# Optimization experiments

Hardware: AMD Instinct MI355X
Metric: run time of the kernel (lower is better)

Reference implementation:

```python
import jax, jax.numpy as jnp
import numpy as np

N = 50000
E = 800000
IN_C, HID_C, OUT_C = 128, 256, 128
BN_EPS = 1e-5


def glorot(key, shape):
    fan_in, fan_out = shape
    lim = float(np.sqrt(6.0 / (fan_in + fan_out)))
    return jax.random.uniform(key, shape, jnp.float32, -lim, lim)


def setup_inputs() -> dict:
    key = jax.random.key(0)
    ks = jax.random.split(key, 16)
    inp = {
        "x": jax.random.normal(ks[0], (N, IN_C), jnp.float32),
        "edge_index": jax.random.randint(ks[1], (2, E), 0, N, jnp.int64),
        # SAGEConv 1 (in->hid): lin_l has bias, lin_r has no bias (PyG default)
        "wl1": glorot(ks[2], (IN_C, HID_C)), "bl1": jnp.zeros((HID_C,), jnp.float32),
        "wr1": glorot(ks[3], (IN_C, HID_C)),
        # SAGEConv 2 (hid->hid)
        "wl2": glorot(ks[4], (HID_C, HID_C)), "bl2": jnp.zeros((HID_C,), jnp.float32),
        "wr2": glorot(ks[5], (HID_C, HID_C)),
        # SAGEConv 3 (hid->out)
        "wl3": glorot(ks[6], (HID_C, OUT_C)), "bl3": jnp.zeros((OUT_C,), jnp.float32),
        "wr3": glorot(ks[7], (HID_C, OUT_C)),
        # BatchNorm params (eval mode: running stats)
        "bn1_w": jnp.ones((HID_C,), jnp.float32), "bn1_b": jnp.zeros((HID_C,), jnp.float32),
        "bn1_m": jax.random.normal(ks[8], (HID_C,), jnp.float32) * 0.1,
        "bn1_v": jax.random.uniform(ks[9], (HID_C,), jnp.float32, 0.5, 1.5),
        "bn2_w": jnp.ones((HID_C,), jnp.float32), "bn2_b": jnp.zeros((HID_C,), jnp.float32),
        "bn2_m": jax.random.normal(ks[10], (HID_C,), jnp.float32) * 0.1,
        "bn2_v": jax.random.uniform(ks[11], (HID_C,), jnp.float32, 0.5, 1.5),
    }
    return inp


def sage_conv(x, src, dst, wl, bl, wr):
    # mean aggregation of source-node features at destination nodes
    agg = jax.ops.segment_sum(x[src], dst, num_segments=N)          # [N, d_in]
    deg = jax.ops.segment_sum(jnp.ones((E,), x.dtype), dst, num_segments=N)
    mean = agg / jnp.maximum(deg, 1.0)[:, None]
    return mean @ wl + bl + x @ wr                                   # [N, d_out]


def batch_norm(x, w, b, m, v):
    return (x - m) * jax.lax.rsqrt(v + BN_EPS) * w + b


def reference(x, edge_index, wl1, bl1, wr1, wl2, bl2, wr2, wl3, bl3, wr3,
              bn1_w, bn1_b, bn1_m, bn1_v, bn2_w, bn2_b, bn2_m, bn2_v):
    src, dst = edge_index[0], edge_index[1]
    # layer 1: SAGEConv -> BN -> ReLU (dropout is identity in eval mode)
    h = sage_conv(x, src, dst, wl1, bl1, wr1)
    h = jax.nn.relu(batch_norm(h, bn1_w, bn1_b, bn1_m, bn1_v))
    # layer 2
    h = sage_conv(h, src, dst, wl2, bl2, wr2)
    h = jax.nn.relu(batch_norm(h, bn2_w, bn2_b, bn2_m, bn2_v))
    # output layer: plain SAGEConv
    return sage_conv(h, src, dst, wl3, bl3, wr3)
```

## Files before the change

### kernel.cpp

```cpp
#include <hip/hip_runtime.h>
#include <hip/hip_bf16.h>

#define NN 50000
#define NE 800000
#define AGG_BLOCKS 2048

typedef __attribute__((ext_vector_type(8))) short bh8;
typedef __attribute__((ext_vector_type(4))) float f32x4;

static __device__ __forceinline__ unsigned short f2bf(float f){
  unsigned u = __float_as_uint(f);
  unsigned r = (u + 0x7fffu + ((u >> 16) & 1u)) >> 16;
  return (unsigned short)r;
}
static __device__ __forceinline__ float bflo(unsigned u){ return __uint_as_float(u << 16); }
static __device__ __forceinline__ float bfhi(unsigned u){ return __uint_as_float(u & 0xffff0000u); }
static __device__ __forceinline__ unsigned packbf2(float lo, float hi){
  return ((unsigned)f2bf(hi) << 16) | (unsigned)f2bf(lo);
}
static __device__ __forceinline__ unsigned char f2fp8(float v){
  return (unsigned char)(__builtin_amdgcn_cvt_pk_fp8_f32(v, v, 0, false) & 0xff);
}

static __device__ __forceinline__ void gload16(const void* g, void* l){
  __builtin_amdgcn_global_load_lds(
      (const __attribute__((address_space(1))) unsigned int*)g,
      (__attribute__((address_space(3))) unsigned int*)l, 16, 0, 0);
}

__global__ __launch_bounds__(256) void pre_k(
    const int* __restrict__ srcv, const int* __restrict__ dstv,
    int* __restrict__ cnt, int* __restrict__ cslot,
    const float4* __restrict__ x, uint2* __restrict__ xb, unsigned* __restrict__ xq,
    const float* __restrict__ wl1, const float* __restrict__ wr1,
    const float* __restrict__ wl2, const float* __restrict__ wr2,
    const float* __restrict__ wl3, const float* __restrict__ wr3,
    const float* __restrict__ bl1, const float* __restrict__ bl2,
    const float* __restrict__ bn1w, const float* __restrict__ bn1b,
    const float* __restrict__ bn1m, const float* __restrict__ bn1v,
    const float* __restrict__ bn2w, const float* __restrict__ bn2b,
    const float* __restrict__ bn2m, const float* __restrict__ bn2v,
    unsigned short* __restrict__ B1t, unsigned short* __restrict__ B2t,
    unsigned short* __restrict__ B3t,
    float* __restrict__ S1, float* __restrict__ T1,
    float* __restrict__ S2, float* __restrict__ T2)
{
  const int blk = blockIdx.x;
  if (blk < 1024){
    const int part  = blk & 3;
    const int chunk = blk >> 2;
    const int lo = part * (NN / 4);
    const int hi = lo + (NN / 4);
    const int base = chunk * (NE / 256);
    const int endi = base + (NE / 256);
    for (int i = base + threadIdx.x; i < endi; i += 256){
      int d = dstv[i];
      if (d >= lo && d < hi){
        int p = atomicAdd(&cnt[d], 1);
        if (p < 64) cslot[(d << 6) + p] = srcv[i];
      }
    }
  } else if (blk < 2050){
    int i = (blk - 1024) * 256 + threadIdx.x;
    if (i < 65536){
      int n = i >> 8, k = i & 255;
      float v = (k < 128) ? wl1[k * 256 + n] : wr1[(k - 128) * 256 + n];
      B1t[n * 256 + k] = f2bf(v);
    } else if (i < 65536 + 131072){
      int j = i - 65536; int n = j >> 9, k = j & 511;
      float v = (k < 256) ? wl2[k * 256 + n] : wr2[(k - 256) * 256 + n];
      B2t[n * 512 + k] = f2bf(v);
    } else if (i < 65536 + 131072 + 65536){
      int j = i - (65536 + 131072); int n = j >> 8, k = j & 255;
      float v = (n < 128) ? wl3[k * 128 + n] : wr3[k * 128 + (n - 128)];
      B3t[n * 256 + k] = f2bf(v);
    } else if (i < 65536 + 131072 + 65536 + 512){
      int j = i - (65536 + 131072 + 65536);
      if (j < 256){
        float s = bn1w[j] * rsqrtf(bn1v[j] + 1e-5f);
        S1[j] = s; T1[j] = (bl1[j] - bn1m[j]) * s + bn1b[j];
      } else {
        int c = j - 256;
        float s = bn2w[c] * rsqrtf(bn2v[c] + 1e-5f);
        S2[c] = s; T2[c] = (bl2[c] - bn2m[c]) * s + bn2b[c];
      }
    }
  } else {
    int i = (blk - 2050) * 256 + threadIdx.x;
    if (i < NN * 128 / 4){
      float4 v = x[i];
      uint2 o; o.x = packbf2(v.x, v.y); o.y = packbf2(v.z, v.w);
      xb[i] = o;
      int w = 0;
      w = __builtin_amdgcn_cvt_pk_fp8_f32(v.x, v.y, w, false);
      w = __builtin_amdgcn_cvt_pk_fp8_f32(v.z, v.w, w, true);
      xq[i] = (unsigned)w;
    }
  }
}

__global__ __launch_bounds__(256) void agg128q_k(const unsigned short* __restrict__ featq,
                         unsigned* __restrict__ out,
                         const int* __restrict__ cnt, const int* __restrict__ cslot){
  const int lane = threadIdx.x & 63;
  const int node0 = __builtin_amdgcn_readfirstlane(blockIdx.x * 4 + (threadIdx.x >> 6));
  const int nw = gridDim.x * 4;
  for (int node = node0; node < NN; node += nw){
    const int start = node << 6;
    const int deg0 = cnt[node];
    const int deg = deg0 < 64 ? deg0 : 64;
    const int end = start + deg;
    float a0 = 0.f, a1 = 0.f, b0 = 0.f, b1 = 0.f;
    int e = start;
    for (; e + 7 < end; e += 8){
      unsigned u0 = featq[(size_t)cslot[e]     * 64 + lane];
      unsigned u1 = featq[(size_t)cslot[e + 1] * 64 + lane];
      unsigned u2 = featq[(size_t)cslot[e + 2] * 64 + lane];
      unsigned u3 = featq[(size_t)cslot[e + 3] * 64 + lane];
      unsigned u4 = featq[(size_t)cslot[e + 4] * 64 + lane];
      unsigned u5 = featq[(size_t)cslot[e + 5] * 64 + lane];
      unsigned u6 = featq[(size_t)cslot[e + 6] * 64 + lane];
      unsigned u7 = featq[(size_t)cslot[e + 7] * 64 + lane];
      a0 += __builtin_amdgcn_cvt_f32_fp8(u0, 0); a1 += __builtin_amdgcn_cvt_f32_fp8(u0, 1);
      b0 += __builtin_amdgcn_cvt_f32_fp8(u1, 0); b1 += __builtin_amdgcn_cvt_f32_fp8(u1, 1);
      a0 += __builtin_amdgcn_cvt_f32_fp8(u2, 0); a1 += __builtin_amdgcn_cvt_f32_fp8(u2, 1);
      b0 += __builtin_amdgcn_cvt_f32_fp8(u3, 0); b1 += __builtin_amdgcn_cvt_f32_fp8(u3, 1);
      a0 += __builtin_amdgcn_cvt_f32_fp8(u4, 0); a1 += __builtin_amdgcn_cvt_f32_fp8(u4, 1);
      b0 += __builtin_amdgcn_cvt_f32_fp8(u5, 0); b1 += __builtin_amdgcn_cvt_f32_fp8(u5, 1);
      a0 += __builtin_amdgcn_cvt_f32_fp8(u6, 0); a1 += __builtin_amdgcn_cvt_f32_fp8(u6, 1);
      b0 += __builtin_amdgcn_cvt_f32_fp8(u7, 0); b1 += __builtin_amdgcn_cvt_f32_fp8(u7, 1);
    }
    for (; e < end; ++e){
      unsigned u = featq[(size_t)cslot[e] * 64 + lane];
      a0 += __builtin_amdgcn_cvt_f32_fp8(u, 0); a1 += __builtin_amdgcn_cvt_f32_fp8(u, 1);
    }
    float inv = 1.f / (float)(deg0 > 0 ? deg0 : 1);
    out[(size_t)node * 64 + lane] = packbf2((a0 + b0) * inv, (a1 + b1) * inv);
  }
}

#define DEC8(u, x0, x1, x2, x3) { \
  x0 += __builtin_amdgcn_cvt_f32_fp8((u), 0); \
  x1 += __builtin_amdgcn_cvt_f32_fp8((u), 1); \
  x2 += __builtin_amdgcn_cvt_f32_fp8((u), 2); \
  x3 += __builtin_amdgcn_cvt_f32_fp8((u), 3); }

__global__ __launch_bounds__(256) void agg256q_k(const unsigned* __restrict__ featq, unsigned* __restrict__ out,
                         const int* __restrict__ cnt, const int* __restrict__ cslot){
  const int lane = threadIdx.x & 63;
  const int node0 = __builtin_amdgcn_readfirstlane(blockIdx.x * 4 + (threadIdx.x >> 6));
  const int nw = gridDim.x * 4;
  for (int node = node0; node < NN; node += nw){
    const int start = node << 6;
    const int deg0 = cnt[node];
    const int deg = deg0 < 64 ? deg0 : 64;
    const int end = start + deg;
    float a0 = 0.f, a1 = 0.f, a2 = 0.f, a3 = 0.f;
    float b0 = 0.f, b1 = 0.f, b2 = 0.f, b3 = 0.f;
    int e = start;
    for (; e + 7 < end; e += 8){
      unsigned u0 = featq[(size_t)cslot[e]     * 64 + lane];
      unsigned u1 = featq[(size_t)cslot[e + 1] * 64 + lane];
      unsigned u2 = featq[(size_t)cslot[e + 2] * 64 + lane];
      unsigned u3 = featq[(size_t)cslot[e + 3] * 64 + lane];
      unsigned u4 = featq[(size_t)cslot[e + 4] * 64 + lane];
      unsigned u5 = featq[(size_t)cslot[e + 5] * 64 + lane];
      unsigned u6 = featq[(size_t)cslot[e + 6] * 64 + lane];
      unsigned u7 = featq[(size_t)cslot[e + 7] * 64 + lane];
      DEC8(u0, a0, a1, a2, a3) DEC8(u1, b0, b1, b2, b3)
      DEC8(u2, a0, a1, a2, a3) DEC8(u3, b0, b1, b2, b3)
      DEC8(u4, a0, a1, a2, a3) DEC8(u5, b0, b1, b2, b3)
      DEC8(u6, a0, a1, a2, a3) DEC8(u7, b0, b1, b2, b3)
    }
    for (; e < end; ++e){
      unsigned u = featq[(size_t)cslot[e] * 64 + lane];
      DEC8(u, a0, a1, a2, a3)
    }
    float inv = 1.f / (float)(deg0 > 0 ? deg0 : 1);
    uint2 o; o.x = packbf2((a0 + b0) * inv, (a1 + b1) * inv);
    o.y = packbf2((a2 + b2) * inv, (a3 + b3) * inv);
    *reinterpret_cast<uint2*>(out + (size_t)node * 128 + lane * 2) = o;
  }
}

__global__ __launch_bounds__(256) void final_k(const unsigned short* __restrict__ tq,
                        const unsigned* __restrict__ ub, float* __restrict__ out,
                        const int* __restrict__ cnt, const int* __restrict__ cslot,
                        const float* __restrict__ bl3){
  const int lane = threadIdx.x & 63;
  const int node0 = __builtin_amdgcn_readfirstlane(blockIdx.x * 4 + (threadIdx.x >> 6));
  const int nw = gridDim.x * 4;
  for (int node = node0; node < NN; node += nw){
    const int start = node << 6;
    const int deg0 = cnt[node];
    const int deg = deg0 < 64 ? deg0 : 64;
    const int end = start + deg;
    float a0 = 0.f, a1 = 0.f, b0 = 0.f, b1 = 0.f;
    int e = start;
    for (; e + 7 < end; e += 8){
      unsigned u0 = tq[(size_t)cslot[e]     * 64 + lane];
      unsigned u1 = tq[(size_t)cslot[e + 1] * 64 + lane];
      unsigned u2 = tq[(size_t)cslot[e + 2] * 64 + lane];
      unsigned u3 = tq[(size_t)cslot[e + 3] * 64 + lane];
      unsigned u4 = tq[(size_t)cslot[e + 4] * 64 + lane];
      unsigned u5 = tq[(size_t)cslot[e + 5] * 64 + lane];
      unsigned u6 = tq[(size_t)cslot[e + 6] * 64 + lane];
      unsigned u7 = tq[(size_t)cslot[e + 7] * 64 + lane];
      a0 += __builtin_amdgcn_cvt_f32_fp8(u0, 0); a1 += __builtin_amdgcn_cvt_f32_fp8(u0, 1);
      b0 += __builtin_amdgcn_cvt_f32_fp8(u1, 0); b1 += __builtin_amdgcn_cvt_f32_fp8(u1, 1);
      a0 += __builtin_amdgcn_cvt_f32_fp8(u2, 0); a1 += __builtin_amdgcn_cvt_f32_fp8(u2, 1);
      b0 += __builtin_amdgcn_cvt_f32_fp8(u3, 0); b1 += __builtin_amdgcn_cvt_f32_fp8(u3, 1);
      a0 += __builtin_amdgcn_cvt_f32_fp8(u4, 0); a1 += __builtin_amdgcn_cvt_f32_fp8(u4, 1);
      b0 += __builtin_amdgcn_cvt_f32_fp8(u5, 0); b1 += __builtin_amdgcn_cvt_f32_fp8(u5, 1);
      a0 += __builtin_amdgcn_cvt_f32_fp8(u6, 0); a1 += __builtin_amdgcn_cvt_f32_fp8(u6, 1);
      b0 += __builtin_amdgcn_cvt_f32_fp8(u7, 0); b1 += __builtin_amdgcn_cvt_f32_fp8(u7, 1);
    }
    for (; e < end; ++e){
      unsigned u = tq[(size_t)cslot[e] * 64 + lane];
      a0 += __builtin_amdgcn_cvt_f32_fp8(u, 0); a1 += __builtin_amdgcn_cvt_f32_fp8(u, 1);
    }
    float inv = 1.f / (float)(deg0 > 0 ? deg0 : 1);
    unsigned uw = ub[(size_t)node * 64 + lane];
    float2 v;
    v.x = bflo(uw) + (a0 + b0) * inv + bl3[lane * 2];
    v.y = bfhi(uw) + (a1 + b1) * inv + bl3[lane * 2 + 1];
    *(reinterpret_cast<float2*>(out + (size_t)node * 128) + lane) = v;
  }
}

template<int KTOT, int K0, int MODE>
__global__ __launch_bounds__(256) void gemm_k(
    const unsigned short* __restrict__ A0, const unsigned short* __restrict__ A1,
    const unsigned short* __restrict__ Bt,
    const float* __restrict__ S, const float* __restrict__ Tt,
    unsigned short* __restrict__ outB, unsigned char* __restrict__ outQ,
    float* __restrict__ outF, int M)
{
  __shared__ __align__(16) unsigned char lds[49152];
  const int tid = threadIdx.x;
  const int lane = tid & 63;
  const int wv = tid >> 6;
  const int wm = wv >> 1, wn = wv & 1;

  const int nwg = gridDim.x;
  const int q = nwg >> 3, r8 = nwg & 7;
  const int xcd = blockIdx.x & 7, idx = blockIdx.x >> 3;
  const int wg = (xcd < r8) ? xcd * (q + 1) + idx : r8 * (q + 1) + (xcd - r8) * q + idx;
  const int bm = wg >> 1, bn = wg & 1;

  const int rr0 = tid >> 2,         g0 = (tid & 3) ^ ((tid >> 3) & 3);
  const int rr1 = (tid + 256) >> 2, g1 = ((tid + 256) & 3) ^ (((tid + 256) >> 3) & 3);
  int growA0 = bm * 128 + rr0; if (growA0 > M - 1) growA0 = M - 1;
  int growA1 = bm * 128 + rr1; if (growA1 > M - 1) growA1 = M - 1;
  const size_t browA0 = (size_t)(bn * 128 + rr0) * KTOT;
  const size_t browA1 = (size_t)(bn * 128 + rr1) * KTOT;

  const int l15 = lane & 15, kg = lane >> 4;
  const int slot = (kg ^ ((l15 >> 1) & 3)) * 16;

  constexpr int NT = KTOT / 32;

  auto STAGE = [&](int buf, int kt){
    const int kb = kt * 32;
    const unsigned short* Ap; int pitch, kk;
    if (KTOT == K0 || kb < K0){ Ap = A0; pitch = K0; kk = kb; }
    else { Ap = A1; pitch = KTOT - K0; kk = kb - K0; }
    unsigned char* base = lds + buf * 16384;
    gload16(Ap + (size_t)growA0 * pitch + kk + g0 * 8, base + tid * 16);
    gload16(Ap + (size_t)growA1 * pitch + kk + g1 * 8, base + 4096 + tid * 16);
    gload16(Bt + browA0 + kb + g0 * 8, base + 8192 + tid * 16);
    gload16(Bt + browA1 + kb + g1 * 8, base + 12288 + tid * 16);
  };

  f32x4 acc[4][4];
  #pragma unroll
  for (int i = 0; i < 4; ++i)
    #pragma unroll
    for (int j = 0; j < 4; ++j){ acc[i][j][0]=0.f; acc[i][j][1]=0.f; acc[i][j][2]=0.f; acc[i][j][3]=0.f; }

  STAGE(0, 0);
  if (NT > 1) STAGE(1, 1);

  int rb = 0, sb = 2;
  for (int kt = 0; kt < NT; ++kt){
    if (kt < NT - 1) asm volatile("s_waitcnt vmcnt(4)" ::: "memory");
    else             asm volatile("s_waitcnt vmcnt(0)" ::: "memory");
    __builtin_amdgcn_s_barrier();
    __builtin_amdgcn_sched_barrier(0);

    if (kt + 2 < NT){ STAGE(sb, kt + 2); sb = (sb == 2) ? 0 : sb + 1; }

    unsigned char* base = lds + rb * 16384;
    rb = (rb == 2) ? 0 : rb + 1;

    bh8 af[4], bf[4];
    #pragma unroll
    for (int mi = 0; mi < 4; ++mi){
      int rA = wm * 64 + mi * 16 + l15;
      af[mi] = *reinterpret_cast<const bh8*>(base + rA * 64 + slot);
    }
    #pragma unroll
    for (int ni = 0; ni < 4; ++ni){
      int rB = wn * 64 + ni * 16 + l15;
      bf[ni] = *reinterpret_cast<const bh8*>(base + 8192 + rB * 64 + slot);
    }
    __builtin_amdgcn_s_setprio(1);
    #pragma unroll
    for (int mi = 0; mi < 4; ++mi)
      #pragma unroll
      for (int ni = 0; ni < 4; ++ni)
        acc[mi][ni] = __builtin_amdgcn_mfma_f32_16x16x32_bf16(af[mi], bf[ni], acc[mi][ni], 0, 0, 0);
    __builtin_amdgcn_s_setprio(0);
  }

  #pragma unroll
  for (int mi = 0; mi < 4; ++mi){
    int rbase = bm * 128 + wm * 64 + mi * 16 + ((lane >> 4) << 2);
    #pragma unroll
    for (int ni = 0; ni < 4; ++ni){
      int col = bn * 128 + wn * 64 + ni * 16 + (lane & 15);
      #pragma unroll
      for (int j = 0; j < 4; ++j){
        int row = rbase + j;
        if (row < M){
          float v = acc[mi][ni][j];
          if (MODE == 0){
            v = v * S[col] + Tt[col];
            v = v > 0.f ? v : 0.f;
            outB[(size_t)row * 256 + col] = f2bf(v);
            if (outQ) outQ[(size_t)row * 256 + col] = f2fp8(v);
          } else {
            if (col < 128) outQ[(size_t)row * 128 + col] = f2fp8(v);
            else           outF[(size_t)row * 128 + (col - 128)] = v;
          }
        }
      }
    }
  }
}

__global__ __launch_bounds__(256) void gemm23_k(
    const unsigned short* __restrict__ A0 ,
    const unsigned short* __restrict__ A1 ,
    const unsigned short* __restrict__ B2 ,
    const unsigned short* __restrict__ B3 ,
    const float* __restrict__ S, const float* __restrict__ Tt,
    unsigned char* __restrict__ tq, unsigned short* __restrict__ ub, int M)
{
  __shared__ __align__(16) unsigned char lds[61440];
  const int tid = threadIdx.x;
  const int lane = tid & 63;
  const int wv = tid >> 6;

  const int nwg = gridDim.x;
  const int q = nwg >> 3, r8 = nwg & 7;
  const int xcd = blockIdx.x & 7, idx = blockIdx.x >> 3;
  const int bm = (xcd < r8) ? xcd * (q + 1) + idx : r8 * (q + 1) + (xcd - r8) * q + idx;

  const int l15 = lane & 15, kg = lane >> 4;
  const int slot = (kg ^ ((l15 >> 1) & 3)) * 16;
  const int rr = tid >> 2;
  const int g  = (tid & 3) ^ ((tid >> 3) & 3);
  int grow = bm * 64 + rr; if (grow > M - 1) grow = M - 1;

  auto STAGE = [&](int buf, int kt){
    const int kb = kt * 32;
    const unsigned short* Ap = (kb < 256) ? A0 : A1;
    const int kk = (kb < 256) ? kb : kb - 256;
    unsigned char* base = lds + buf * 20480;
    gload16(Ap + (size_t)grow * 256 + kk + g * 8, base + tid * 16);
    gload16(B2 + (size_t)(rr      ) * 512 + kb + g * 8, base +  4096 + tid * 16);
    gload16(B2 + (size_t)(rr +  64) * 512 + kb + g * 8, base +  8192 + tid * 16);
    gload16(B2 + (size_t)(rr + 128) * 512 + kb + g * 8, base + 12288 + tid * 16);
    gload16(B2 + (size_t)(rr + 192) * 512 + kb + g * 8, base + 16384 + tid * 16);
  };

  f32x4 acc[4][4];
  #pragma unroll
  for (int i = 0; i < 4; ++i)
    #pragma unroll
    for (int j = 0; j < 4; ++j){ acc[i][j][0]=0.f; acc[i][j][1]=0.f; acc[i][j][2]=0.f; acc[i][j][3]=0.f; }

  STAGE(0, 0);
  STAGE(1, 1);

  int rb = 0, sb = 2;
  #pragma unroll 1
  for (int kt = 0; kt < 16; ++kt){
    if (kt < 15) asm volatile("s_waitcnt vmcnt(5)" ::: "memory");
    else         asm volatile("s_waitcnt vmcnt(0)" ::: "memory");
    __builtin_amdgcn_s_barrier();
    __builtin_amdgcn_sched_barrier(0);

    if (kt + 2 < 16){ STAGE(sb, kt + 2); sb = (sb == 2) ? 0 : sb + 1; }

    unsigned char* base = lds + rb * 20480;
    rb = (rb == 2) ? 0 : rb + 1;

    bh8 af[4], bf[4];
    #pragma unroll
    for (int mi = 0; mi < 4; ++mi)
      af[mi] = *reinterpret_cast<const bh8*>(base + (mi * 16 + l15) * 64 + slot);
    #pragma unroll
    for (int ni = 0; ni < 4; ++ni)
      bf[ni] = *reinterpret_cast<const bh8*>(base + 4096 + (wv * 64 + ni * 16 + l15) * 64 + slot);

    __builtin_amdgcn_s_setprio(1);
    #pragma unroll
    for (int mi = 0; mi < 4; ++mi)
      #pragma unroll
      for (int ni = 0; ni < 4; ++ni)
        acc[mi][ni] = __builtin_amdgcn_mfma_f32_16x16x32_bf16(bf[ni], af[mi], acc[mi][ni], 0, 0, 0);
    __builtin_amdgcn_s_setprio(0);
  }

  __syncthreads();
  #pragma unroll
  for (int mi = 0; mi < 4; ++mi){
    const int row = mi * 16 + l15;
    #pragma unroll
    for (int ni = 0; ni < 4; ++ni){
      const int c0 = wv * 64 + ni * 16 + kg * 4;
      float v0 = acc[mi][ni][0] * S[c0]     + Tt[c0];     v0 = v0 > 0.f ? v0 : 0.f;
      float v1 = acc[mi][ni][1] * S[c0 + 1] + Tt[c0 + 1]; v1 = v1 > 0.f ? v1 : 0.f;
      float v2 = acc[mi][ni][2] * S[c0 + 2] + Tt[c0 + 2]; v2 = v2 > 0.f ? v2 : 0.f;
      float v3 = acc[mi][ni][3] * S[c0 + 3] + Tt[c0 + 3]; v3 = v3 > 0.f ? v3 : 0.f;
      uint2 w; w.x = packbf2(v0, v1); w.y = packbf2(v2, v3);
      const int chunk = wv * 8 + ni * 2 + (kg >> 1);
      const int byte = row * 512 + ((chunk ^ (row & 7)) * 16) + (kg & 1) * 8;
      *reinterpret_cast<uint2*>(lds + byte) = w;
    }
  }
  __syncthreads();

  f32x4 acc2[4][4];
  #pragma unroll
  for (int i = 0; i < 4; ++i)
    #pragma unroll
    for (int j = 0; j < 4; ++j){ acc2[i][j][0]=0.f; acc2[i][j][1]=0.f; acc2[i][j][2]=0.f; acc2[i][j][3]=0.f; }

  #pragma unroll 1
  for (int kt = 0; kt < 8; ++kt){
    const int kb = kt * 32;
    bh8 af2[4], bf2[4];
    #pragma unroll
    for (int mi = 0; mi < 4; ++mi){
      const int row = mi * 16 + l15;
      const int chunk = kt * 4 + kg;
      af2[mi] = *reinterpret_cast<const bh8*>(lds + row * 512 + ((chunk ^ (row & 7)) * 16));
    }
    #pragma unroll
    for (int ni = 0; ni < 4; ++ni)
      bf2[ni] = *reinterpret_cast<const bh8*>(B3 + (size_t)(wv * 64 + ni * 16 + l15) * 256 + kb + kg * 8);
    __builtin_amdgcn_s_setprio(1);
    #pragma unroll
    for (int mi = 0; mi < 4; ++mi)
      #pragma unroll
      for (int ni = 0; ni < 4; ++ni)
        acc2[mi][ni] = __builtin_amdgcn_mfma_f32_16x16x32_bf16(af2[mi], bf2[ni], acc2[mi][ni], 0, 0, 0);
    __builtin_amdgcn_s_setprio(0);
  }

  #pragma unroll
  for (int mi = 0; mi < 4; ++mi){
    const int rbase = bm * 64 + mi * 16 + (kg << 2);
    #pragma unroll
    for (int ni = 0; ni < 4; ++ni){
      const int col = wv * 64 + ni * 16 + l15;
      #pragma unroll
      for (int j = 0; j < 4; ++j){
        const int row = rbase + j;
        if (row < M){
          float v = acc2[mi][ni][j];
          if (col < 128) tq[(size_t)row * 128 + col] = f2fp8(v);
          else           ub[(size_t)row * 128 + (col - 128)] = f2bf(v);
        }
      }
    }
  }
}

extern "C" void kernel_launch(void* const* d_in, const int* in_sizes, int n_in,
                              void* d_out, int out_size, void* d_ws, size_t ws_size,
                              hipStream_t stream) {
  (void)in_sizes; (void)n_in; (void)out_size; (void)ws_size;
  const float* x   = (const float*)d_in[0];
  const int*   ei  = (const int*)d_in[1];
  const int*   srcv = ei;
  const int*   dstv = ei + NE;
  const float* wl1 = (const float*)d_in[2];
  const float* bl1 = (const float*)d_in[3];
  const float* wr1 = (const float*)d_in[4];
  const float* wl2 = (const float*)d_in[5];
  const float* bl2 = (const float*)d_in[6];
  const float* wr2 = (const float*)d_in[7];
  const float* wl3 = (const float*)d_in[8];
  const float* bl3 = (const float*)d_in[9];
  const float* wr3 = (const float*)d_in[10];
  const float* bn1w = (const float*)d_in[11];
  const float* bn1b = (const float*)d_in[12];
  const float* bn1m = (const float*)d_in[13];
  const float* bn1v = (const float*)d_in[14];
  const float* bn2w = (const float*)d_in[15];
  const float* bn2b = (const float*)d_in[16];
  const float* bn2m = (const float*)d_in[17];
  const float* bn2v = (const float*)d_in[18];

  char* ws = (char*)d_ws;
  size_t off = 0;
  auto alloc = [&](size_t bytes) -> void* {
    void* p = ws + off;
    off += (bytes + 255) & ~(size_t)255;
    return p;
  };
  int* cnt   = (int*)alloc((size_t)NN * 4);
  int* cslot = (int*)alloc((size_t)NN * 64 * 4);
  unsigned short* B1t = (unsigned short*)alloc(256 * 256 * 2);
  unsigned short* B2t = (unsigned short*)alloc(256 * 512 * 2);
  unsigned short* B3t = (unsigned short*)alloc(256 * 256 * 2);
  float* S1 = (float*)alloc(256 * 4);
  float* T1 = (float*)alloc(256 * 4);
  float* S2 = (float*)alloc(256 * 4);
  float* T2 = (float*)alloc(256 * 4);
  unsigned short* xb   = (unsigned short*)alloc((size_t)NN * 128 * 2);
  unsigned short* agg1 = (unsigned short*)alloc((size_t)NN * 128 * 2);
  unsigned short* h1   = (unsigned short*)alloc((size_t)NN * 256 * 2);
  unsigned short* h2   = (unsigned short*)alloc((size_t)NN * 256 * 2);
  unsigned short* agg2 = xb;
  unsigned char*  h1q  = (unsigned char*)h2;
  unsigned*       xq   = (unsigned*)((unsigned char*)h2 + (size_t)NN * 256);
  unsigned char*  tq   = (unsigned char*)h2;
  unsigned short* ub   = (unsigned short*)((unsigned char*)h2 + (size_t)NN * 256);
  float* outp = (float*)d_out;

  hipMemsetAsync(cnt, 0, (size_t)NN * 4, stream);
  pre_k<<<8300, 256, 0, stream>>>(srcv, dstv, cnt, cslot,
                                  (const float4*)x, (uint2*)xb, xq,
                                  wl1, wr1, wl2, wr2, wl3, wr3, bl1, bl2,
                                  bn1w, bn1b, bn1m, bn1v, bn2w, bn2b, bn2m, bn2v,
                                  B1t, B2t, B3t, S1, T1, S2, T2);

  agg128q_k<<<AGG_BLOCKS, 256, 0, stream>>>((const unsigned short*)xq, (unsigned*)agg1, cnt, cslot);
  gemm_k<256, 128, 0><<<782, 256, 0, stream>>>(agg1, xb, B1t, S1, T1, h1, h1q, nullptr, NN);
  agg256q_k<<<AGG_BLOCKS, 256, 0, stream>>>((const unsigned*)h1q, (unsigned*)agg2, cnt, cslot);
  gemm23_k<<<782, 256, 0, stream>>>(agg2, h1, B2t, B3t, S2, T2, tq, ub, NN);
  final_k<<<AGG_BLOCKS, 256, 0, stream>>>((const unsigned short*)tq, (const unsigned*)ub, outp, cnt, cslot, bl3);
}
```

Baseline: 220.4 us.

## Fuse layer-2 gather aggregation into the layer-2/3 GEMM kernel

Removes the separate agg256q_k kernel and has gemm23f_k gather and average FP8 neighbour features straight into LDS, alongside the node's own bf16 h1 row, as the full A tile. The M tile shrinks from 64 to 32 rows, so the grid doubles to 1563 blocks, and LDS grows to hold the whole 32x512 A tile plus triple-buffered B. The goal is to drop the agg2 write and read-back and one launch. The cost is that gather latency now sits inside the GEMM blocks before any MFMA work starts, B tiles are re-read once per smaller M tile, and the larger LDS footprint may lower occupancy. Output buffers tq and ub are moved into other workspace regions to avoid aliasing h1q.

```diff
diff --git a/kernel.cpp b/kernel.cpp
--- a/kernel.cpp
+++ b/kernel.cpp
@@ -145,44 +145,6 @@
   x2 += __builtin_amdgcn_cvt_f32_fp8((u), 2); \
   x3 += __builtin_amdgcn_cvt_f32_fp8((u), 3); }
 
-__global__ __launch_bounds__(256) void agg256q_k(const unsigned* __restrict__ featq, unsigned* __restrict__ out,
-                         const int* __restrict__ cnt, const int* __restrict__ cslot){
-  const int lane = threadIdx.x & 63;
-  const int node0 = __builtin_amdgcn_readfirstlane(blockIdx.x * 4 + (threadIdx.x >> 6));
-  const int nw = gridDim.x * 4;
-  for (int node = node0; node < NN; node += nw){
-    const int start = node << 6;
-    const int deg0 = cnt[node];
-    const int deg = deg0 < 64 ? deg0 : 64;
-    const int end = start + deg;
-    float a0 = 0.f, a1 = 0.f, a2 = 0.f, a3 = 0.f;
-    float b0 = 0.f, b1 = 0.f, b2 = 0.f, b3 = 0.f;
-    int e = start;
-    for (; e + 7 < end; e += 8){
-      unsigned u0 = featq[(size_t)cslot[e]     * 64 + lane];
-      unsigned u1 = featq[(size_t)cslot[e + 1] * 64 + lane];
-      unsigned u2 = featq[(size_t)cslot[e + 2] * 64 + lane];
-      unsigned u3 = featq[(size_t)cslot[e + 3] * 64 + lane];
-      unsigned u4 = featq[(size_t)cslot[e + 4] * 64 + lane];
-      unsigned u5 = featq[(size_t)cslot[e + 5] * 64 + lane];
-      unsigned u6 = featq[(size_t)cslot[e + 6] * 64 + lane];
-      unsigned u7 = featq[(size_t)cslot[e + 7] * 64 + lane];
-      DEC8(u0, a0, a1, a2, a3) DEC8(u1, b0, b1, b2, b3)
-      DEC8(u2, a0, a1, a2, a3) DEC8(u3, b0, b1, b2, b3)
-      DEC8(u4, a0, a1, a2, a3) DEC8(u5, b0, b1, b2, b3)
-      DEC8(u6, a0, a1, a2, a3) DEC8(u7, b0, b1, b2, b3)
-    }
-    for (; e < end; ++e){
-      unsigned u = featq[(size_t)cslot[e] * 64 + lane];
-      DEC8(u, a0, a1, a2, a3)
-    }
-    float inv = 1.f / (float)(deg0 > 0 ? deg0 : 1);
-    uint2 o; o.x = packbf2((a0 + b0) * inv, (a1 + b1) * inv);
-    o.y = packbf2((a2 + b2) * inv, (a3 + b3) * inv);
-    *reinterpret_cast<uint2*>(out + (size_t)node * 128 + lane * 2) = o;
-  }
-}
-
 __global__ __launch_bounds__(256) void final_k(const unsigned short* __restrict__ tq,
                         const unsigned* __restrict__ ub, float* __restrict__ out,
                         const int* __restrict__ cnt, const int* __restrict__ cslot,
@@ -339,15 +301,16 @@
   }
 }
 
-__global__ __launch_bounds__(256) void gemm23_k(
-    const unsigned short* __restrict__ A0 ,
-    const unsigned short* __restrict__ A1 ,
+__global__ __launch_bounds__(256) void gemm23f_k(
+    const int* __restrict__ cnt, const int* __restrict__ cslot,
+    const unsigned* __restrict__ h1q ,
+    const unsigned short* __restrict__ h1 ,
     const unsigned short* __restrict__ B2 ,
     const unsigned short* __restrict__ B3 ,
     const float* __restrict__ S, const float* __restrict__ Tt,
     unsigned char* __restrict__ tq, unsigned short* __restrict__ ub, int M)
 {
-  __shared__ __align__(16) unsigned char lds[61440];
+  __shared__ __align__(16) unsigned char lds[81920];
   const int tid = threadIdx.x;
   const int lane = tid & 63;
   const int wv = tid >> 6;
@@ -361,53 +324,96 @@
   const int slot = (kg ^ ((l15 >> 1) & 3)) * 16;
   const int rr = tid >> 2;
   const int g  = (tid & 3) ^ ((tid >> 3) & 3);
-  int grow = bm * 64 + rr; if (grow > M - 1) grow = M - 1;
-
-  auto STAGE = [&](int buf, int kt){
+
+  auto STAGE_B = [&](int buf, int kt){
     const int kb = kt * 32;
-    const unsigned short* Ap = (kb < 256) ? A0 : A1;
-    const int kk = (kb < 256) ? kb : kb - 256;
-    unsigned char* base = lds + buf * 20480;
-    gload16(Ap + (size_t)grow * 256 + kk + g * 8, base + tid * 16);
-    gload16(B2 + (size_t)(rr      ) * 512 + kb + g * 8, base +  4096 + tid * 16);
-    gload16(B2 + (size_t)(rr +  64) * 512 + kb + g * 8, base +  8192 + tid * 16);
-    gload16(B2 + (size_t)(rr + 128) * 512 + kb + g * 8, base + 12288 + tid * 16);
-    gload16(B2 + (size_t)(rr + 192) * 512 + kb + g * 8, base + 16384 + tid * 16);
+    unsigned char* base = lds + 32768 + buf * 16384;
+    gload16(B2 + (size_t)(rr      ) * 512 + kb + g * 8, base +         tid * 16);
+    gload16(B2 + (size_t)(rr +  64) * 512 + kb + g * 8, base +  4096 + tid * 16);
+    gload16(B2 + (size_t)(rr + 128) * 512 + kb + g * 8, base +  8192 + tid * 16);
+    gload16(B2 + (size_t)(rr + 192) * 512 + kb + g * 8, base + 12288 + tid * 16);
   };
 
-  f32x4 acc[4][4];
+  STAGE_B(0, 0);
+  STAGE_B(1, 1);
+
+  for (int i = 0; i < 8; ++i){
+    const int r = wv * 8 + i;
+    int node = bm * 32 + r; if (node > M - 1) node = M - 1;
+    {
+      uint2 w = *reinterpret_cast<const uint2*>(h1 + (size_t)node * 256 + lane * 4);
+      const int c = 32 + (lane >> 1);
+      const int byte = r * 1024 + ((c ^ (r & 7)) * 16) + (lane & 1) * 8;
+      *reinterpret_cast<uint2*>(lds + byte) = w;
+    }
+    {
+      const int deg0 = cnt[node];
+      const int deg = deg0 < 64 ? deg0 : 64;
+      const int start = node << 6;
+      const int end = start + deg;
+      float a0 = 0.f, a1 = 0.f, a2 = 0.f, a3 = 0.f;
+      float b0 = 0.f, b1 = 0.f, b2 = 0.f, b3 = 0.f;
+      int e = start;
+      for (; e + 7 < end; e += 8){
+        unsigned u0 = h1q[(size_t)cslot[e]     * 64 + lane];
+        unsigned u1 = h1q[(size_t)cslot[e + 1] * 64 + lane];
+        unsigned u2 = h1q[(size_t)cslot[e + 2] * 64 + lane];
+        unsigned u3 = h1q[(size_t)cslot[e + 3] * 64 + lane];
+        unsigned u4 = h1q[(size_t)cslot[e + 4] * 64 + lane];
+        unsigned u5 = h1q[(size_t)cslot[e + 5] * 64 + lane];
+        unsigned u6 = h1q[(size_t)cslot[e + 6] * 64 + lane];
+        unsigned u7 = h1q[(size_t)cslot[e + 7] * 64 + lane];
+        DEC8(u0, a0, a1, a2, a3) DEC8(u1, b0, b1, b2, b3)
+        DEC8(u2, a0, a1, a2, a3) DEC8(u3, b0, b1, b2, b3)
+        DEC8(u4, a0, a1, a2, a3) DEC8(u5, b0, b1, b2, b3)
+        DEC8(u6, a0, a1, a2, a3) DEC8(u7, b0, b1, b2, b3)
+      }
+      for (; e < end; ++e){
+        unsigned u = h1q[(size_t)cslot[e] * 64 + lane];
+        DEC8(u, a0, a1, a2, a3)
+      }
+      float inv = 1.f / (float)(deg0 > 0 ? deg0 : 1);
+      uint2 w;
+      w.x = packbf2((a0 + b0) * inv, (a1 + b1) * inv);
+      w.y = packbf2((a2 + b2) * inv, (a3 + b3) * inv);
+      const int c = lane >> 1;
+      const int byte = r * 1024 + ((c ^ (r & 7)) * 16) + (lane & 1) * 8;
+      *reinterpret_cast<uint2*>(lds + byte) = w;
+    }
+  }
+  __syncthreads();
+
+  f32x4 acc[2][4];
   #pragma unroll
-  for (int i = 0; i < 4; ++i)
+  for (int i = 0; i < 2; ++i)
     #pragma unroll
     for (int j = 0; j < 4; ++j){ acc[i][j][0]=0.f; acc[i][j][1]=0.f; acc[i][j][2]=0.f; acc[i][j][3]=0.f; }
 
-  STAGE(0, 0);
-  STAGE(1, 1);
-
-  int rb = 0, sb = 2;
   #pragma unroll 1
   for (int kt = 0; kt < 16; ++kt){
-    if (kt < 15) asm volatile("s_waitcnt vmcnt(5)" ::: "memory");
+    if (kt < 15) asm volatile("s_waitcnt vmcnt(4)" ::: "memory");
     else         asm volatile("s_waitcnt vmcnt(0)" ::: "memory");
     __builtin_amdgcn_s_barrier();
     __builtin_amdgcn_sched_barrier(0);
 
-    if (kt + 2 < 16){ STAGE(sb, kt + 2); sb = (sb == 2) ? 0 : sb + 1; }
-
-    unsigned char* base = lds + rb * 20480;
-    rb = (rb == 2) ? 0 : rb + 1;
-
-    bh8 af[4], bf[4];
-    #pragma unroll
-    for (int mi = 0; mi < 4; ++mi)
-      af[mi] = *reinterpret_cast<const bh8*>(base + (mi * 16 + l15) * 64 + slot);
+    if (kt + 2 < 16) STAGE_B((kt + 2) % 3, kt + 2);
+
+    unsigned char* bbase = lds + 32768 + (kt % 3) * 16384;
+
+    bh8 af[2], bf[4];
+    #pragma unroll
+    for (int mi = 0; mi < 2; ++mi){
+      const int row = mi * 16 + l15;
+      const int c = kt * 4 + kg;
+      af[mi] = *reinterpret_cast<const bh8*>(lds + row * 1024 + ((c ^ (row & 7)) * 16));
+    }
     #pragma unroll
     for (int ni = 0; ni < 4; ++ni)
-      bf[ni] = *reinterpret_cast<const bh8*>(base + 4096 + (wv * 64 + ni * 16 + l15) * 64 + slot);
+      bf[ni] = *reinterpret_cast<const bh8*>(bbase + (wv * 64 + ni * 16 + l15) * 64 + slot);
 
     __builtin_amdgcn_s_setprio(1);
     #pragma unroll
-    for (int mi = 0; mi < 4; ++mi)
+    for (int mi = 0; mi < 2; ++mi)
       #pragma unroll
       for (int ni = 0; ni < 4; ++ni)
         acc[mi][ni] = __builtin_amdgcn_mfma_f32_16x16x32_bf16(bf[ni], af[mi], acc[mi][ni], 0, 0, 0);
@@ -416,7 +422,7 @@
 
   __syncthreads();
   #pragma unroll
-  for (int mi = 0; mi < 4; ++mi){
+  for (int mi = 0; mi < 2; ++mi){
     const int row = mi * 16 + l15;
     #pragma unroll
     for (int ni = 0; ni < 4; ++ni){
@@ -433,18 +439,18 @@
   }
   __syncthreads();
 
-  f32x4 acc2[4][4];
+  f32x4 acc2[2][4];
   #pragma unroll
-  for (int i = 0; i < 4; ++i)
+  for (int i = 0; i < 2; ++i)
     #pragma unroll
     for (int j = 0; j < 4; ++j){ acc2[i][j][0]=0.f; acc2[i][j][1]=0.f; acc2[i][j][2]=0.f; acc2[i][j][3]=0.f; }
 
   #pragma unroll 1
   for (int kt = 0; kt < 8; ++kt){
     const int kb = kt * 32;
-    bh8 af2[4], bf2[4];
-    #pragma unroll
-    for (int mi = 0; mi < 4; ++mi){
+    bh8 af2[2], bf2[4];
+    #pragma unroll
+    for (int mi = 0; mi < 2; ++mi){
       const int row = mi * 16 + l15;
       const int chunk = kt * 4 + kg;
       af2[mi] = *reinterpret_cast<const bh8*>(lds + row * 512 + ((chunk ^ (row & 7)) * 16));
@@ -454,7 +460,7 @@
       bf2[ni] = *reinterpret_cast<const bh8*>(B3 + (size_t)(wv * 64 + ni * 16 + l15) * 256 + kb + kg * 8);
     __builtin_amdgcn_s_setprio(1);
     #pragma unroll
-    for (int mi = 0; mi < 4; ++mi)
+    for (int mi = 0; mi < 2; ++mi)
       #pragma unroll
       for (int ni = 0; ni < 4; ++ni)
         acc2[mi][ni] = __builtin_amdgcn_mfma_f32_16x16x32_bf16(af2[mi], bf2[ni], acc2[mi][ni], 0, 0, 0);
@@ -462,8 +468,8 @@
   }
 
   #pragma unroll
-  for (int mi = 0; mi < 4; ++mi){
-    const int rbase = bm * 64 + mi * 16 + (kg << 2);
+  for (int mi = 0; mi < 2; ++mi){
+    const int rbase = bm * 32 + mi * 16 + (kg << 2);
     #pragma unroll
     for (int ni = 0; ni < 4; ++ni){
       const int col = wv * 64 + ni * 16 + l15;
@@ -526,11 +532,10 @@
   unsigned short* agg1 = (unsigned short*)alloc((size_t)NN * 128 * 2);
   unsigned short* h1   = (unsigned short*)alloc((size_t)NN * 256 * 2);
   unsigned short* h2   = (unsigned short*)alloc((size_t)NN * 256 * 2);
-  unsigned short* agg2 = xb;
   unsigned char*  h1q  = (unsigned char*)h2;
   unsigned*       xq   = (unsigned*)((unsigned char*)h2 + (size_t)NN * 256);
-  unsigned char*  tq   = (unsigned char*)h2;
-  unsigned short* ub   = (unsigned short*)((unsigned char*)h2 + (size_t)NN * 256);
+  unsigned char*  tq   = (unsigned char*)agg1;
+  unsigned short* ub   = xb;
   float* outp = (float*)d_out;
 
   hipMemsetAsync(cnt, 0, (size_t)NN * 4, stream);
@@ -542,7 +547,7 @@
 
   agg128q_k<<<AGG_BLOCKS, 256, 0, stream>>>((const unsigned short*)xq, (unsigned*)agg1, cnt, cslot);
   gemm_k<256, 128, 0><<<782, 256, 0, stream>>>(agg1, xb, B1t, S1, T1, h1, h1q, nullptr, NN);
-  agg256q_k<<<AGG_BLOCKS, 256, 0, stream>>>((const unsigned*)h1q, (unsigned*)agg2, cnt, cslot);
-  gemm23_k<<<782, 256, 0, stream>>>(agg2, h1, B2t, B3t, S2, T2, tq, ub, NN);
+  gemm23f_k<<<1563, 256, 0, stream>>>(cnt, cslot, (const unsigned*)h1q, h1,
+                                      B2t, B3t, S2, T2, tq, ub, NN);
   final_k<<<AGG_BLOCKS, 256, 0, stream>>>((const unsigned short*)tq, (const unsigned*)ub, outp, cnt, cslot, bl3);
 }
```

Result: slower. 306.9 us (+39.3%).
